# Kernel optimization log

Measured on AMD Instinct MI355X. Metric: run time of the kernel, lower is better.

The kernel has to match this reference:

```python
import jax, jax.numpy as jnp
import numpy as np

N_NODES = 50000


def gcn_conv(x, W, b, src, dst, n_nodes):
    # Linear transform first (PyG GCNConv): [N, out]
    h = x @ W
    # Add self-loops
    loop = jnp.arange(n_nodes, dtype=src.dtype)
    s = jnp.concatenate([src, loop])
    d = jnp.concatenate([dst, loop])
    # Symmetric normalization: deg counted at destination with unit weights
    deg = jax.ops.segment_sum(jnp.ones_like(d, dtype=h.dtype), d, num_segments=n_nodes)
    dinv = jnp.where(deg > 0, jax.lax.rsqrt(deg), 0.0)
    norm = dinv[s] * dinv[d]  # [E+N]
    # Gather source features, scale, scatter-add to destinations
    msgs = h[s] * norm[:, None]
    out = jax.ops.segment_sum(msgs, d, num_segments=n_nodes)
    return out + b


def setup_inputs() -> dict:
    key = jax.random.key(0)
    k1, k2, k3, k4, k5 = jax.random.split(key, 5)
    in_c, out_c = 512, 128
    x = jax.random.normal(k1, (N_NODES, in_c), dtype=jnp.float32)
    edge_index = jax.random.randint(k2, (2, 800000), 0, N_NODES, dtype=jnp.int64)
    glorot = 1.0 / np.sqrt(in_c)
    W_mu = jax.random.uniform(k3, (in_c, out_c), jnp.float32, -glorot, glorot)
    W_logstd = jax.random.uniform(k4, (in_c, out_c), jnp.float32, -glorot, glorot)
    b_mu = jnp.zeros((out_c,), jnp.float32)
    b_logstd = jnp.zeros((out_c,), jnp.float32)
    return {"x": x, "edge_index": edge_index, "W_mu": W_mu, "b_mu": b_mu,
            "W_logstd": W_logstd, "b_logstd": b_logstd}


def reference(x, edge_index, W_mu, b_mu, W_logstd, b_logstd):
    src, dst = edge_index[0], edge_index[1]
    mu = gcn_conv(x, W_mu, b_mu, src, dst, N_NODES)
    logstd = gcn_conv(x, W_logstd, b_logstd, src, dst, N_NODES)
    return mu, logstd
```

## Files before the change

### kernel.cpp

```cpp
#include <hip/hip_runtime.h>

#define NN 50000
#define NE 800000
#define KC 512
#define OC 256
#define NB_SCAN 196

typedef float f32x4 __attribute__((ext_vector_type(4)));
typedef short bf16x8 __attribute__((ext_vector_type(8)));

__device__ __forceinline__ unsigned f2bf(float f) {
    union { float f; unsigned u; } v; v.f = f;
    return (v.u + 0x7FFFu + ((v.u >> 16) & 1u)) >> 16;
}
__device__ __forceinline__ float bf2f(unsigned short b) {
    union { unsigned u; float f; } v; v.u = ((unsigned)b) << 16;
    return v.f;
}

__global__ __launch_bounds__(256) void count_deg_kernel(const int* __restrict__ ei,
                                                        int* __restrict__ deg) {
    int e = blockIdx.x * 256 + threadIdx.x;
    if (e < NE) atomicAdd(&deg[ei[NE + e]], 1);
}

__global__ __launch_bounds__(256) void scan_part_kernel(const int* __restrict__ deg,
                                                        int* __restrict__ partial) {
    int tid = threadIdx.x;
    int i = blockIdx.x * 256 + tid;
    int v = (i < NN) ? deg[i] : 0;
#pragma unroll
    for (int off = 32; off > 0; off >>= 1) v += __shfl_down(v, off, 64);
    __shared__ int wsum[4];
    if ((tid & 63) == 0) wsum[tid >> 6] = v;
    __syncthreads();
    if (tid == 0) partial[blockIdx.x] = wsum[0] + wsum[1] + wsum[2] + wsum[3];
}

__global__ __launch_bounds__(256) void scan_block_kernel(const int* __restrict__ partial,
                                                         int* __restrict__ blockoff) {
    __shared__ int lds[256];
    int tid = threadIdx.x;
    int v = (tid < NB_SCAN) ? partial[tid] : 0;
    lds[tid] = v;
    __syncthreads();
    for (int off = 1; off < 256; off <<= 1) {
        int t = (tid >= off) ? lds[tid - off] : 0;
        __syncthreads();
        lds[tid] += t;
        __syncthreads();
    }
    if (tid < NB_SCAN) blockoff[tid] = lds[tid] - v;
}

__global__ __launch_bounds__(256) void scan_apply_kernel(const int* __restrict__ deg,
                                                         const int* __restrict__ blockoff,
                                                         int* __restrict__ row_start,
                                                         int* __restrict__ cursor,
                                                         float* __restrict__ dinv) {
    int tid = threadIdx.x;
    int lane = tid & 63;
    int w = tid >> 6;
    int i = blockIdx.x * 256 + tid;
    int d = (i < NN) ? deg[i] : 0;
    int v = d;
#pragma unroll
    for (int off = 1; off < 64; off <<= 1) {
        int t = __shfl_up(v, off, 64);
        if (lane >= off) v += t;
    }
    __shared__ int wsum[4];
    if (lane == 63) wsum[w] = v;
    __syncthreads();
    int wof = 0;
    for (int k = 0; k < w; ++k) wof += wsum[k];
    int excl = blockoff[blockIdx.x] + wof + v - d;
    if (i < NN) {
        row_start[i] = excl;
        cursor[i] = excl;
        dinv[i] = rsqrtf((float)(d + 1));
    }
    if (i == NN - 1) row_start[NN] = excl + d;
}

__global__ __launch_bounds__(256) void scatter_kernel(const int* __restrict__ ei,
                                                      int* __restrict__ cursor,
                                                      int* __restrict__ csr_src) {
    int e = blockIdx.x * 256 + threadIdx.x;
    if (e < NE) {
        int d = ei[NE + e];
        int pos = atomicAdd(&cursor[d], 1);
        csr_src[pos] = ei[e];
    }
}

__global__ __launch_bounds__(256) void convw_kernel(const float* __restrict__ Wmu,
                                                    const float* __restrict__ Wls,
                                                    uint4* __restrict__ Wc) {
    int idx = blockIdx.x * 256 + threadIdx.x;
    int kb = idx >> 10;
    int rem = idx & 1023;
    int wf = rem >> 6;
    int lane = rem & 63;
    int g4 = lane >> 4;
    int i16 = lane & 15;
    int col = (wf >> 2) * 64 + (wf & 3) * 16 + i16;
    int k0 = kb * 32 + g4 * 8;
    const float* Wsrc = (col < 128) ? (Wmu + col) : (Wls + (col - 128));
    unsigned o[4];
#pragma unroll
    for (int p = 0; p < 4; ++p) {
        float lo = Wsrc[(size_t)(k0 + 2 * p) * 128];
        float hi = Wsrc[(size_t)(k0 + 2 * p + 1) * 128];
        o[p] = f2bf(lo) | (f2bf(hi) << 16);
    }
    uint4 v;
    v.x = o[0]; v.y = o[1]; v.z = o[2]; v.w = o[3];
    Wc[idx] = v;
}

#define ALD 136
__global__ __launch_bounds__(256, 4) void gemm_kernel(const float* __restrict__ x,
                                                      const uint4* __restrict__ Wc,
                                                      const float* __restrict__ dinv,
                                                      unsigned short* __restrict__ hs) {
    __shared__ __align__(16) unsigned short As[2][32 * ALD];

    int tid = threadIdx.x;
    int lane = tid & 63;
    int w = tid >> 6;
    int r0 = blockIdx.x * 32;
    int i16 = lane & 15;
    int g4 = lane >> 4;

    int st_row = tid >> 3;
    int st_c = tid & 7;
    int xr = r0 + st_row;
    if (xr > NN - 1) xr = NN - 1;
    const float* xg = x + (size_t)xr * KC + st_c * 16;
    unsigned short* adst = &As[0][st_row * ALD + st_c * 16];

    float4 xa[4];
    auto loadA = [&](int S) {
#pragma unroll
        for (int i = 0; i < 4; ++i) xa[i] = *(const float4*)(xg + S * 128 + i * 4);
    };
    auto storeA = [&](int buf) {
        uint4* dst = (uint4*)(adst + buf * 32 * ALD);
#pragma unroll
        for (int p = 0; p < 2; ++p) {
            uint4 o;
            o.x = f2bf(xa[2 * p].x) | (f2bf(xa[2 * p].y) << 16);
            o.y = f2bf(xa[2 * p].z) | (f2bf(xa[2 * p].w) << 16);
            o.z = f2bf(xa[2 * p + 1].x) | (f2bf(xa[2 * p + 1].y) << 16);
            o.w = f2bf(xa[2 * p + 1].z) | (f2bf(xa[2 * p + 1].w) << 16);
            dst[p] = o;
        }
    };

    const uint4* wbase = Wc + (size_t)(w * 4) * 64 + lane;
    uint4 bb[2][4];
    auto loadB = [&](int dbuf, int kb) {
#pragma unroll
        for (int fc = 0; fc < 4; ++fc) bb[dbuf][fc] = wbase[kb * 1024 + fc * 64];
    };

    f32x4 acc[2][4];
    f32x4 zz = {0.f, 0.f, 0.f, 0.f};
#pragma unroll
    for (int a = 0; a < 2; ++a)
#pragma unroll
        for (int b = 0; b < 4; ++b) acc[a][b] = zz;

    loadA(0);
    storeA(0);
    __syncthreads();
    loadA(1);
    loadB(0, 0);

#pragma unroll
    for (int S = 0; S < 4; ++S) {
#pragma unroll
        for (int ks = 0; ks < 4; ++ks) {
            const int kb = S * 4 + ks;
            const int cur = kb & 1;
            if (kb < 15) loadB(cur ^ 1, kb + 1);
            bf16x8 af[2];
#pragma unroll
            for (int fr = 0; fr < 2; ++fr)
                af[fr] = *(const bf16x8*)&As[S & 1][(fr * 16 + i16) * ALD + ks * 32 + g4 * 8];
#pragma unroll
            for (int fc = 0; fc < 4; ++fc) {
                bf16x8 bfrag = *(const bf16x8*)&bb[cur][fc];
#pragma unroll
                for (int fr = 0; fr < 2; ++fr)
                    acc[fr][fc] = __builtin_amdgcn_mfma_f32_16x16x32_bf16(af[fr], bfrag, acc[fr][fc], 0, 0, 0);
            }
        }
        if (S < 3) {
            storeA((S + 1) & 1);
            __syncthreads();
            if (S < 2) loadA(S + 2);
        }
    }

#pragma unroll
    for (int fr = 0; fr < 2; ++fr) {
#pragma unroll
        for (int r = 0; r < 4; ++r) {
            int gr = r0 + fr * 16 + g4 * 4 + r;
            if (gr < NN) {
                float dv = dinv[gr];
#pragma unroll
                for (int fc = 0; fc < 4; ++fc) {
                    int col = w * 64 + fc * 16 + i16;
                    hs[(size_t)gr * OC + col] = (unsigned short)f2bf(acc[fr][fc][r] * dv);
                }
            }
        }
    }
}

__global__ __launch_bounds__(256) void aggregate_kernel(const unsigned short* __restrict__ hs,
                                                        const int* __restrict__ row_start,
                                                        const int* __restrict__ csr_src,
                                                        const float* __restrict__ dinv,
                                                        const float* __restrict__ bmu,
                                                        const float* __restrict__ bls,
                                                        float* __restrict__ out) {
    int tid = threadIdx.x;
    int lane = tid & 63;
    int node = blockIdx.x * 4 + (tid >> 6);

    const unsigned short* hrow = hs + lane * 4;
    float acc0, acc1, acc2, acc3;
    {
        ushort4 v = *(const ushort4*)&hrow[(size_t)node * OC];
        acc0 = bf2f(v.x);
        acc1 = bf2f(v.y);
        acc2 = bf2f(v.z);
        acc3 = bf2f(v.w);
    }
    int rs = row_start[node], re = row_start[node + 1];
    int e = rs;
    for (; e + 8 <= re; e += 8) {
        int s[8];
#pragma unroll
        for (int q = 0; q < 8; ++q) s[q] = csr_src[e + q];
        ushort4 v[8];
#pragma unroll
        for (int q = 0; q < 8; ++q) v[q] = *(const ushort4*)&hrow[(size_t)s[q] * OC];
#pragma unroll
        for (int q = 0; q < 8; ++q) {
            acc0 += bf2f(v[q].x);
            acc1 += bf2f(v[q].y);
            acc2 += bf2f(v[q].z);
            acc3 += bf2f(v[q].w);
        }
    }
    if (e + 4 <= re) {
        int s[4];
#pragma unroll
        for (int q = 0; q < 4; ++q) s[q] = csr_src[e + q];
        ushort4 v[4];
#pragma unroll
        for (int q = 0; q < 4; ++q) v[q] = *(const ushort4*)&hrow[(size_t)s[q] * OC];
#pragma unroll
        for (int q = 0; q < 4; ++q) {
            acc0 += bf2f(v[q].x);
            acc1 += bf2f(v[q].y);
            acc2 += bf2f(v[q].z);
            acc3 += bf2f(v[q].w);
        }
        e += 4;
    }
    for (; e < re; ++e) {
        int s0 = csr_src[e];
        ushort4 v0 = *(const ushort4*)&hrow[(size_t)s0 * OC];
        acc0 += bf2f(v0.x);
        acc1 += bf2f(v0.y);
        acc2 += bf2f(v0.z);
        acc3 += bf2f(v0.w);
    }
    float dn = dinv[node];
    if (lane < 32) {
        float4 b = ((const float4*)bmu)[lane];
        float4 r = {acc0 * dn + b.x, acc1 * dn + b.y, acc2 * dn + b.z, acc3 * dn + b.w};
        ((float4*)out)[(size_t)node * 32 + lane] = r;
    } else {
        float4 b = ((const float4*)bls)[lane - 32];
        float4 r = {acc0 * dn + b.x, acc1 * dn + b.y, acc2 * dn + b.z, acc3 * dn + b.w};
        ((float4*)out)[(size_t)(NN + node) * 32 + (lane - 32)] = r;
    }
}

extern "C" void kernel_launch(void* const* d_in, const int* in_sizes, int n_in,
                              void* d_out, int out_size, void* d_ws, size_t ws_size,
                              hipStream_t stream) {
    const float* x = (const float*)d_in[0];
    const int* ei = (const int*)d_in[1];
    const float* Wmu = (const float*)d_in[2];
    const float* bmu = (const float*)d_in[3];
    const float* Wls = (const float*)d_in[4];
    const float* bls = (const float*)d_in[5];
    float* out = (float*)d_out;

    char* ws = (char*)d_ws;
    size_t off = 0;
    auto alloc = [&](size_t bytes) {
        void* p = ws + off;
        off += (bytes + 255) & ~(size_t)255;
        return p;
    };
    unsigned short* hs = (unsigned short*)alloc((size_t)NN * OC * sizeof(unsigned short));
    uint4* Wc = (uint4*)alloc((size_t)16384 * 16);
    int* deg = (int*)alloc((size_t)NN * sizeof(int));
    int* row_start = (int*)alloc((size_t)(NN + 1) * sizeof(int));
    int* cursor = (int*)alloc((size_t)NN * sizeof(int));
    int* csr_src = (int*)alloc((size_t)NE * sizeof(int));
    float* dinv = (float*)alloc((size_t)NN * sizeof(float));
    int* partial = (int*)alloc((size_t)NB_SCAN * sizeof(int));
    int* blockoff = (int*)alloc((size_t)NB_SCAN * sizeof(int));

    hipMemsetAsync(deg, 0, (size_t)NN * sizeof(int), stream);

    count_deg_kernel<<<(NE + 255) / 256, 256, 0, stream>>>(ei, deg);
    scan_part_kernel<<<NB_SCAN, 256, 0, stream>>>(deg, partial);
    scan_block_kernel<<<1, 256, 0, stream>>>(partial, blockoff);
    scan_apply_kernel<<<NB_SCAN, 256, 0, stream>>>(deg, blockoff, row_start, cursor, dinv);
    scatter_kernel<<<(NE + 255) / 256, 256, 0, stream>>>(ei, cursor, csr_src);
    convw_kernel<<<64, 256, 0, stream>>>(Wmu, Wls, Wc);
    gemm_kernel<<<(NN + 31) / 32, 256, 0, stream>>>(x, Wc, dinv, hs);
    aggregate_kernel<<<NN / 4, 256, 0, stream>>>(hs, row_start, csr_src, dinv, bmu, bls, out);
}
```

Measured before the change: 200.6 us.

## Store GEMM output column-chunked and aggregate per 32-column slice

The GEMM now writes h in a chunked layout: 8 column slabs, each NN x 32 bf16 (64 bytes per node row). The aggregation kernel gets a 2D grid with one slab per blockIdx.y and 16 lanes per node, each lane handling two columns. This is meant to shrink the working set per slab (50000 x 64 bytes) so the random gathers hit cache better. The cost is that the CSR indices and row offsets are re-read 8 times and each gather is a narrower 64-byte segment.

```diff
diff --git a/kernel.cpp b/kernel.cpp
--- a/kernel.cpp
+++ b/kernel.cpp
@@ -16,6 +16,13 @@
 __device__ __forceinline__ float bf2f(unsigned short b) {
     union { unsigned u; float f; } v; v.u = ((unsigned)b) << 16;
     return v.f;
+}
+__device__ __forceinline__ void unpack2(unsigned v, float& lo, float& hi) {
+    union { unsigned u; float f; } a, b;
+    a.u = v << 16;
+    b.u = v & 0xffff0000u;
+    lo = a.f;
+    hi = b.f;
 }
 
 __global__ __launch_bounds__(256) void count_deg_kernel(const int* __restrict__ ei,
@@ -123,7 +130,7 @@
 __global__ __launch_bounds__(256, 4) void gemm_kernel(const float* __restrict__ x,
                                                       const uint4* __restrict__ Wc,
                                                       const float* __restrict__ dinv,
-                                                      unsigned short* __restrict__ hs) {
+                                                      unsigned short* __restrict__ hsC) {
     __shared__ __align__(16) unsigned short As[2][32 * ALD];
 
     int tid = threadIdx.x;
@@ -214,14 +221,15 @@
 #pragma unroll
                 for (int fc = 0; fc < 4; ++fc) {
                     int col = w * 64 + fc * 16 + i16;
-                    hs[(size_t)gr * OC + col] = (unsigned short)f2bf(acc[fr][fc][r] * dv);
+                    hsC[((size_t)(col >> 5) * NN + gr) * 32 + (col & 31)] =
+                        (unsigned short)f2bf(acc[fr][fc][r] * dv);
                 }
             }
         }
     }
 }
 
-__global__ __launch_bounds__(256) void aggregate_kernel(const unsigned short* __restrict__ hs,
+__global__ __launch_bounds__(256) void aggregate_kernel(const unsigned short* __restrict__ hsC,
                                                         const int* __restrict__ row_start,
                                                         const int* __restrict__ csr_src,
                                                         const float* __restrict__ dinv,
@@ -229,17 +237,15 @@
                                                         const float* __restrict__ bls,
                                                         float* __restrict__ out) {
     int tid = threadIdx.x;
-    int lane = tid & 63;
-    int node = blockIdx.x * 4 + (tid >> 6);
-
-    const unsigned short* hrow = hs + lane * 4;
-    float acc0, acc1, acc2, acc3;
+    int c = blockIdx.y;
+    int g16 = tid & 15;
+    int node = blockIdx.x * 16 + (tid >> 4);
+
+    const unsigned short* base = hsC + (size_t)c * NN * 32 + g16 * 2;
+    float a0, a1;
     {
-        ushort4 v = *(const ushort4*)&hrow[(size_t)node * OC];
-        acc0 = bf2f(v.x);
-        acc1 = bf2f(v.y);
-        acc2 = bf2f(v.z);
-        acc3 = bf2f(v.w);
+        unsigned v = *(const unsigned*)&base[(size_t)node * 32];
+        unpack2(v, a0, a1);
     }
     int rs = row_start[node], re = row_start[node + 1];
     int e = rs;
@@ -247,51 +253,53 @@
         int s[8];
 #pragma unroll
         for (int q = 0; q < 8; ++q) s[q] = csr_src[e + q];
-        ushort4 v[8];
-#pragma unroll
-        for (int q = 0; q < 8; ++q) v[q] = *(const ushort4*)&hrow[(size_t)s[q] * OC];
+        unsigned v[8];
+#pragma unroll
+        for (int q = 0; q < 8; ++q) v[q] = *(const unsigned*)&base[(size_t)s[q] * 32];
 #pragma unroll
         for (int q = 0; q < 8; ++q) {
-            acc0 += bf2f(v[q].x);
-            acc1 += bf2f(v[q].y);
-            acc2 += bf2f(v[q].z);
-            acc3 += bf2f(v[q].w);
+            float f0, f1;
+            unpack2(v[q], f0, f1);
+            a0 += f0;
+            a1 += f1;
         }
     }
     if (e + 4 <= re) {
         int s[4];
 #pragma unroll
         for (int q = 0; q < 4; ++q) s[q] = csr_src[e + q];
-        ushort4 v[4];
-#pragma unroll
-        for (int q = 0; q < 4; ++q) v[q] = *(const ushort4*)&hrow[(size_t)s[q] * OC];
+        unsigned v[4];
+#pragma unroll
+        for (int q = 0; q < 4; ++q) v[q] = *(const unsigned*)&base[(size_t)s[q] * 32];
 #pragma unroll
         for (int q = 0; q < 4; ++q) {
-            acc0 += bf2f(v[q].x);
-            acc1 += bf2f(v[q].y);
-            acc2 += bf2f(v[q].z);
-            acc3 += bf2f(v[q].w);
+            float f0, f1;
+            unpack2(v[q], f0, f1);
+            a0 += f0;
+            a1 += f1;
         }
         e += 4;
     }
     for (; e < re; ++e) {
-        int s0 = csr_src[e];
-        ushort4 v0 = *(const ushort4*)&hrow[(size_t)s0 * OC];
-        acc0 += bf2f(v0.x);
-        acc1 += bf2f(v0.y);
-        acc2 += bf2f(v0.z);
-        acc3 += bf2f(v0.w);
+        unsigned v = *(const unsigned*)&base[(size_t)csr_src[e] * 32];
+        float f0, f1;
+        unpack2(v, f0, f1);
+        a0 += f0;
+        a1 += f1;
     }
     float dn = dinv[node];
-    if (lane < 32) {
-        float4 b = ((const float4*)bmu)[lane];
-        float4 r = {acc0 * dn + b.x, acc1 * dn + b.y, acc2 * dn + b.z, acc3 * dn + b.w};
-        ((float4*)out)[(size_t)node * 32 + lane] = r;
+    int col = c * 32 + g16 * 2;
+    float2 b;
+    float* outp;
+    if (c < 4) {
+        b = *(const float2*)&bmu[col];
+        outp = out + (size_t)node * 128 + col;
     } else {
-        float4 b = ((const float4*)bls)[lane - 32];
-        float4 r = {acc0 * dn + b.x, acc1 * dn + b.y, acc2 * dn + b.z, acc3 * dn + b.w};
-        ((float4*)out)[(size_t)(NN + node) * 32 + (lane - 32)] = r;
-    }
+        b = *(const float2*)&bls[col - 128];
+        outp = out + (size_t)NN * 128 + (size_t)node * 128 + (col - 128);
+    }
+    float2 r = {a0 * dn + b.x, a1 * dn + b.y};
+    *(float2*)outp = r;
 }
 
 extern "C" void kernel_launch(void* const* d_in, const int* in_sizes, int n_in,
@@ -312,7 +320,7 @@
         off += (bytes + 255) & ~(size_t)255;
         return p;
     };
-    unsigned short* hs = (unsigned short*)alloc((size_t)NN * OC * sizeof(unsigned short));
+    unsigned short* hsC = (unsigned short*)alloc((size_t)NN * OC * sizeof(unsigned short));
     uint4* Wc = (uint4*)alloc((size_t)16384 * 16);
     int* deg = (int*)alloc((size_t)NN * sizeof(int));
     int* row_start = (int*)alloc((size_t)(NN + 1) * sizeof(int));
@@ -330,6 +338,7 @@
     scan_apply_kernel<<<NB_SCAN, 256, 0, stream>>>(deg, blockoff, row_start, cursor, dinv);
     scatter_kernel<<<(NE + 255) / 256, 256, 0, stream>>>(ei, cursor, csr_src);
     convw_kernel<<<64, 256, 0, stream>>>(Wmu, Wls, Wc);
-    gemm_kernel<<<(NN + 31) / 32, 256, 0, stream>>>(x, Wc, dinv, hs);
-    aggregate_kernel<<<NN / 4, 256, 0, stream>>>(hs, row_start, csr_src, dinv, bmu, bls, out);
-}
+    gemm_kernel<<<(NN + 31) / 32, 256, 0, stream>>>(x, Wc, dinv, hsC);
+    dim3 agrid(NN / 16, 8);
+    aggregate_kernel<<<agrid, 256, 0, stream>>>(hsC, row_start, csr_src, dinv, bmu, bls, out);
+}
```

Measured after the change: 215.9 us. +7.7%, slower.
